# Optimization experiments

Measured on AMD Instinct MI355X. Metric: run time of the kernel, lower is better.

The kernel has to match this reference:

```python
import jax, jax.numpy as jnp
import numpy as np

B, N, D, D_OUT = 8, 2048, 256, 256
LN_EPS = 1e-5
LRELU_SLOPE = 0.01


def setup_inputs() -> dict:
    key = jax.random.key(0)
    ks = jax.random.split(key, 11)
    s_in = 1.0 / np.sqrt(D)
    s_out = 1.0 / np.sqrt(D)
    return {
        "x_local": jax.random.normal(ks[0], (B, N, D), dtype=jnp.float32),
        "Wq": jax.random.uniform(ks[1], (D, D), jnp.float32, -s_in, s_in),
        "bq": jax.random.uniform(ks[2], (D,), jnp.float32, -s_in, s_in),
        "Wk": jax.random.uniform(ks[3], (D, D), jnp.float32, -s_in, s_in),
        "bk": jax.random.uniform(ks[4], (D,), jnp.float32, -s_in, s_in),
        "Wv": jax.random.uniform(ks[5], (D, D), jnp.float32, -s_in, s_in),
        "bv": jax.random.uniform(ks[6], (D,), jnp.float32, -s_in, s_in),
        "Wo": jax.random.uniform(ks[7], (D_OUT, D), jnp.float32, -s_out, s_out),
        "bo": jax.random.uniform(ks[8], (D_OUT,), jnp.float32, -s_out, s_out),
        "ln_gamma": jnp.ones((D_OUT,), jnp.float32),
        "ln_beta": jnp.zeros((D_OUT,), jnp.float32),
    }


def reference(x_local, Wq, bq, Wk, bk, Wv, bv, Wo, bo, ln_gamma, ln_beta):
    # Linear layers (torch convention: y = x @ W.T + b)
    Q = jnp.einsum("bnd,ed->bne", x_local, Wq) + bq
    K = jnp.einsum("bnd,ed->bne", x_local, Wk) + bk
    V = jnp.einsum("bnd,ed->bne", x_local, Wv) + bv
    # Unscaled attention (source applies no 1/sqrt(d))
    scores = jnp.einsum("bnd,bmd->bnm", Q, K)          # [B, N, N]
    attn = jax.nn.softmax(scores, axis=-1)
    loc = jnp.einsum("bnm,bmd->bnd", attn, V)           # [B, N, D]
    # fc_out: Linear -> LayerNorm -> LeakyReLU
    h = jnp.einsum("bnd,ed->bne", loc, Wo) + bo          # [B, N, D_OUT]
    mu = jnp.mean(h, axis=-1, keepdims=True)
    var = jnp.mean(jnp.square(h - mu), axis=-1, keepdims=True)
    hn = (h - mu) / jnp.sqrt(var + LN_EPS) * ln_gamma + ln_beta
    return jnp.where(hn >= 0, hn, LRELU_SLOPE * hn)
```

## Files before the change

### kernel.cpp

```cpp
#include <hip/hip_runtime.h>

typedef unsigned short u16;
typedef __attribute__((ext_vector_type(8))) _Float16 f16x8;
typedef __attribute__((ext_vector_type(4))) float f32x4;

#define MFMA_F16 __builtin_amdgcn_mfma_f32_16x16x32_f16

static __device__ __forceinline__ u16 f2h(float f) {
    return __builtin_bit_cast(u16, (_Float16)f);
}
static __device__ __forceinline__ ushort4 f4_to_h4(const float4 v) {
    ushort4 r;
    r.x = f2h(v.x); r.y = f2h(v.y); r.z = f2h(v.z); r.w = f2h(v.w);
    return r;
}

__global__ __launch_bounds__(256) void prep_w(
    const float* __restrict__ wq, const float* __restrict__ wk,
    const float* __restrict__ wv, const float* __restrict__ wo,
    u16* __restrict__ w4)
{
    const int tid = blockIdx.x * 256 + threadIdx.x;
    for (int i = tid; i < 65536; i += 16384) {
        const float* src = (i < 16384) ? wq : (i < 32768) ? wk
                         : (i < 49152) ? wv : wo;
        ((ushort4*)w4)[i] = f4_to_h4(((const float4*)src)[i & 16383]);
    }
}

__global__ __launch_bounds__(256) void proj_qkv(
    const float* __restrict__ X, const u16* __restrict__ w4,
    const float* __restrict__ bq, const float* __restrict__ bk,
    const float* __restrict__ bv,
    u16* __restrict__ Qh, u16* __restrict__ Kh, u16* __restrict__ Vt)
{
    const int z = blockIdx.y;
    const u16* __restrict__ W     = w4 + z * 65536;
    const float* __restrict__ bias = (z == 0) ? bq : (z == 1) ? bk : bv;

    const int m0   = blockIdx.x * 64;
    const int t    = threadIdx.x;
    const int w    = t >> 6;
    const int lane = t & 63;
    const int quad = lane >> 4;
    const int l16  = lane & 15;

    __shared__ __align__(16) u16 smem[18432];
    u16* Xs = smem;
    u16* Ws = smem + 2560;

    f32x4 acc[16];
#pragma unroll
    for (int i = 0; i < 16; ++i) acc[i] = f32x4{0.f, 0.f, 0.f, 0.f};

    for (int kc = 0; kc < 8; ++kc) {
#pragma unroll
        for (int i = 0; i < 2; ++i) {
            const int ch = i * 256 + t;
            const int row = ch >> 3, cg = ch & 7;
            const float4 v = *(const float4*)&X[(size_t)(m0 + row) * 256 + kc * 32 + cg * 4];
            *(ushort4*)&Xs[row * 40 + cg * 4] = f4_to_h4(v);
        }
#pragma unroll
        for (int i = 0; i < 4; ++i) {
            const int ch = i * 256 + t;
            const int row = ch >> 2, cg = ch & 3;
            *(int4*)&Ws[row * 40 + cg * 8] =
                *(const int4*)&W[(size_t)row * 256 + kc * 32 + cg * 8];
        }
        __syncthreads();

        const f16x8 af = *(const f16x8*)&Xs[(w * 16 + l16) * 40 + quad * 8];
#pragma unroll
        for (int nt = 0; nt < 16; ++nt) {
            const f16x8 bf = *(const f16x8*)&Ws[(nt * 16 + l16) * 40 + quad * 8];
            acc[nt] = MFMA_F16(af, bf, acc[nt], 0, 0, 0);
        }
        __syncthreads();
    }

    if (z < 2) {
        u16* __restrict__ Y = (z == 0) ? Qh : Kh;
#pragma unroll
        for (int nt = 0; nt < 16; ++nt) {
            const int col = nt * 16 + l16;
            const float bb = bias[col];
#pragma unroll
            for (int r = 0; r < 4; ++r)
                smem[(w * 16 + quad * 4 + r) * 264 + col] = f2h(acc[nt][r] + bb);
        }
        __syncthreads();
#pragma unroll
        for (int i = 0; i < 8; ++i) {
            const int ch = i * 256 + t;
            const int row = ch >> 5, cg = ch & 31;
            *(int4*)&Y[(size_t)(m0 + row) * 256 + cg * 8] =
                *(const int4*)&smem[row * 264 + cg * 8];
        }
    } else {
        const int b  = m0 >> 11;
        const int n0 = m0 & 2047;
#pragma unroll
        for (int nt = 0; nt < 16; ++nt) {
            const int col = nt * 16 + l16;
            const float bb = bias[col];
            ushort4 h4;
            h4.x = f2h(acc[nt][0] + bb);
            h4.y = f2h(acc[nt][1] + bb);
            h4.z = f2h(acc[nt][2] + bb);
            h4.w = f2h(acc[nt][3] + bb);
            *(ushort4*)&smem[col * 72 + w * 16 + quad * 4] = h4;
        }
        __syncthreads();
#pragma unroll
        for (int i = 0; i < 8; ++i) {
            const int ch = i * 256 + t;
            const int row = ch >> 3, cg = ch & 7;
            *(int4*)&Vt[(size_t)b * 524288 + (size_t)row * 2048 + n0 + cg * 8] =
                *(const int4*)&smem[row * 72 + cg * 8];
        }
    }
}

__global__ __launch_bounds__(256) void attn(
    const u16* __restrict__ Qh, const u16* __restrict__ Kg,
    const u16* __restrict__ Vt, u16* __restrict__ Op, float* __restrict__ lmp)
{
    const int nz = gridDim.z;
    const int z  = blockIdx.z;
    const int tbase = 64 / nz, trem = 64 % nz;
    const int my_tiles = tbase + (z < trem ? 1 : 0);
    const int tile0    = tbase * z + (z < trem ? z : trem);

    const int b  = blockIdx.y;
    const int q0 = blockIdx.x * 64;
    const int t    = threadIdx.x;
    const int w    = t >> 6;
    const int lane = t & 63;
    const int quad = lane >> 4;
    const int l16  = lane & 15;

    __shared__ __align__(16) u16 smem[18688];
    u16* Ks = smem;
    u16* Vs = smem + 8448;
    u16* Os = smem;

    f16x8 qf[8];
    {
        const size_t qrow = (size_t)(b * 2048 + q0 + w * 16 + l16) * 256;
#pragma unroll
        for (int kc = 0; kc < 8; ++kc)
            qf[kc] = *(const f16x8*)&Qh[qrow + kc * 32 + quad * 8];
    }

    f32x4 O[16];
#pragma unroll
    for (int i = 0; i < 16; ++i) O[i] = f32x4{0.f, 0.f, 0.f, 0.f};
    float mrow = -1e30f, lrow = 0.f;

    for (int it = 0; it < my_tiles; ++it) {
        const int kt = (tile0 + it) * 32;
#pragma unroll
        for (int i = 0; i < 4; ++i) {
            const int ch = i * 256 + t;
            const int row = ch >> 5, cg = ch & 31;
            const int prow = ((row >> 2) & 3) * 8 + (row >> 4) * 4 + (row & 3);
            *(int4*)&Ks[row * 264 + cg * 8] =
                *(const int4*)&Kg[(size_t)(b * 2048 + kt + prow) * 256 + cg * 8];
        }
#pragma unroll
        for (int i = 0; i < 4; ++i) {
            const int ch = i * 256 + t;
            const int row = ch >> 2, cg = ch & 3;
            *(int4*)&Vs[row * 40 + cg * 8] =
                *(const int4*)&Vt[(size_t)b * 524288 + (size_t)row * 2048 + kt + cg * 8];
        }
        __syncthreads();

        f32x4 S[2];
        S[0] = f32x4{0.f, 0.f, 0.f, 0.f};
        S[1] = f32x4{0.f, 0.f, 0.f, 0.f};
#pragma unroll
        for (int kc = 0; kc < 8; ++kc) {
#pragma unroll
            for (int kn = 0; kn < 2; ++kn) {
                const f16x8 kf = *(const f16x8*)&Ks[(kn * 16 + l16) * 264 + kc * 32 + quad * 8];
                S[kn] = MFMA_F16(kf, qf[kc], S[kn], 0, 0, 0);
            }
        }

        float mt = fmaxf(fmaxf(fmaxf(S[0][0], S[0][1]), fmaxf(S[0][2], S[0][3])),
                         fmaxf(fmaxf(S[1][0], S[1][1]), fmaxf(S[1][2], S[1][3])));
        mt = fmaxf(mt, __shfl_xor(mt, 16));
        mt = fmaxf(mt, __shfl_xor(mt, 32));
        const float mnew = fmaxf(mrow, mt);
        const float a = __expf(mrow - mnew);
        float p[2][4];
        float s = 0.f;
#pragma unroll
        for (int kn = 0; kn < 2; ++kn)
#pragma unroll
            for (int r = 0; r < 4; ++r) {
                p[kn][r] = __expf(S[kn][r] - mnew);
                s += p[kn][r];
            }
        s += __shfl_xor(s, 16);
        s += __shfl_xor(s, 32);
        lrow = a * lrow + s;
        mrow = mnew;

        if (__any(a < 1.f)) {
#pragma unroll
            for (int dv = 0; dv < 16; ++dv)
#pragma unroll
                for (int r = 0; r < 4; ++r) O[dv][r] *= a;
        }

        f16x8 pf;
#pragma unroll
        for (int kn = 0; kn < 2; ++kn)
#pragma unroll
            for (int r = 0; r < 4; ++r)
                pf[kn * 4 + r] = (_Float16)p[kn][r];

#pragma unroll
        for (int dvt = 0; dvt < 16; ++dvt) {
            const f16x8 vf = *(const f16x8*)&Vs[(dvt * 16 + l16) * 40 + quad * 8];
            O[dvt] = MFMA_F16(vf, pf, O[dvt], 0, 0, 0);
        }
        __syncthreads();
    }

    {
        const float rl = 1.0f / lrow;
#pragma unroll
        for (int dvt = 0; dvt < 16; ++dvt) {
            ushort4 h4;
            h4.x = f2h(O[dvt][0] * rl);
            h4.y = f2h(O[dvt][1] * rl);
            h4.z = f2h(O[dvt][2] * rl);
            h4.w = f2h(O[dvt][3] * rl);
            *(ushort4*)&Os[(w * 16 + l16) * 264 + dvt * 16 + quad * 4] = h4;
        }
        if (quad == 0) {
            const int grow = b * 2048 + q0 + w * 16 + l16;
            lmp[z * 16384 + grow]        = lrow;
            lmp[(nz + z) * 16384 + grow] = mrow;
        }
    }
    __syncthreads();

    u16* __restrict__ Oz = Op + (size_t)z * 4194304;
    {
        const int row = t >> 2;
#pragma unroll
        for (int i = 0; i < 8; ++i) {
            const int chunk = (t & 3) * 8 + i;
            *(int4*)&Oz[(size_t)(b * 2048 + q0 + row) * 256 + chunk * 8] =
                *(const int4*)&Os[row * 264 + chunk * 8];
        }
    }
}

__global__ __launch_bounds__(256) void outproj_ln(
    const u16* __restrict__ Op, const float* __restrict__ lmp,
    const u16* __restrict__ Woh, const float* __restrict__ bo,
    const float* __restrict__ gamma, const float* __restrict__ beta,
    float* __restrict__ out)
{
    const int m0   = blockIdx.x * 64;
    const int t    = threadIdx.x;
    const int w    = t >> 6;
    const int lane = t & 63;
    const int quad = lane >> 4;
    const int l16  = lane & 15;

    __shared__ __align__(16) u16 Ls[64 * 40];
    __shared__ __align__(16) u16 Ws[256 * 40];
    __shared__ _Float16 w0s[64], w1s[64];

    if (t < 64) {
        const float l0 = lmp[m0 + t],          l1 = lmp[16384 + m0 + t];
        const float mm0 = lmp[32768 + m0 + t], mm1 = lmp[49152 + m0 + t];
        const float mm = fmaxf(mm0, mm1);
        const float u0 = l0 * __expf(mm0 - mm);
        const float u1 = l1 * __expf(mm1 - mm);
        const float inv = 1.0f / (u0 + u1);
        w0s[t] = (_Float16)(u0 * inv);
        w1s[t] = (_Float16)(u1 * inv);
    }
    __syncthreads();

    f32x4 acc[16];
#pragma unroll
    for (int i = 0; i < 16; ++i) acc[i] = f32x4{0.f, 0.f, 0.f, 0.f};

    for (int kc = 0; kc < 8; ++kc) {
        {
            const int row = t >> 2, cg = t & 3;
            const size_t off = (size_t)(m0 + row) * 256 + kc * 32 + cg * 8;
            const f16x8 o0 = __builtin_bit_cast(f16x8, *(const int4*)&Op[off]);
            const f16x8 o1 = __builtin_bit_cast(f16x8, *(const int4*)&Op[4194304 + off]);
            const _Float16 w0 = w0s[row], w1 = w1s[row];
            f16x8 lw;
#pragma unroll
            for (int j = 0; j < 8; ++j) lw[j] = o0[j] * w0 + o1[j] * w1;
            *(int4*)&Ls[row * 40 + cg * 8] = __builtin_bit_cast(int4, lw);
        }
#pragma unroll
        for (int i = 0; i < 4; ++i) {
            const int ch = i * 256 + t;
            const int row = ch >> 2, cg = ch & 3;
            *(int4*)&Ws[row * 40 + cg * 8] =
                *(const int4*)&Woh[(size_t)row * 256 + kc * 32 + cg * 8];
        }
        __syncthreads();

        const f16x8 af = *(const f16x8*)&Ls[(w * 16 + l16) * 40 + quad * 8];
#pragma unroll
        for (int nt = 0; nt < 16; ++nt) {
            const f16x8 bf = *(const f16x8*)&Ws[(nt * 16 + l16) * 40 + quad * 8];
            acc[nt] = MFMA_F16(af, bf, acc[nt], 0, 0, 0);
        }
        __syncthreads();
    }

    float g[16], bt[16], bb[16];
#pragma unroll
    for (int nt = 0; nt < 16; ++nt) {
        const int col = nt * 16 + l16;
        bb[nt] = bo[col]; g[nt] = gamma[col]; bt[nt] = beta[col];
    }

#pragma unroll
    for (int r = 0; r < 4; ++r) {
        float h[16];
        float sh = 0.f, sh2 = 0.f;
#pragma unroll
        for (int nt = 0; nt < 16; ++nt) {
            h[nt] = acc[nt][r] + bb[nt];
            sh  += h[nt];
            sh2 += h[nt] * h[nt];
        }
        sh  += __shfl_xor(sh, 1);  sh  += __shfl_xor(sh, 2);
        sh  += __shfl_xor(sh, 4);  sh  += __shfl_xor(sh, 8);
        sh2 += __shfl_xor(sh2, 1); sh2 += __shfl_xor(sh2, 2);
        sh2 += __shfl_xor(sh2, 4); sh2 += __shfl_xor(sh2, 8);
        const float mu  = sh * (1.f / 256.f);
        const float var = fmaxf(sh2 * (1.f / 256.f) - mu * mu, 0.f);
        const float rs  = rsqrtf(var + 1e-5f);
        const size_t row = (size_t)(m0 + w * 16 + quad * 4 + r) * 256;
#pragma unroll
        for (int nt = 0; nt < 16; ++nt) {
            const float hn = (h[nt] - mu) * rs * g[nt] + bt[nt];
            out[row + nt * 16 + l16] = (hn >= 0.f) ? hn : 0.01f * hn;
        }
    }
}

extern "C" void kernel_launch(void* const* d_in, const int* in_sizes, int n_in,
                              void* d_out, int out_size, void* d_ws, size_t ws_size,
                              hipStream_t stream)
{
    const float* x  = (const float*)d_in[0];
    const float* Wq = (const float*)d_in[1];
    const float* bq = (const float*)d_in[2];
    const float* Wk = (const float*)d_in[3];
    const float* bk = (const float*)d_in[4];
    const float* Wv = (const float*)d_in[5];
    const float* bv = (const float*)d_in[6];
    const float* Wo = (const float*)d_in[7];
    const float* bo = (const float*)d_in[8];
    const float* gm = (const float*)d_in[9];
    const float* bt = (const float*)d_in[10];
    float* out = (float*)d_out;

    u16* W4 = (u16*)d_ws;
    u16* Qh = W4 + 262144;
    u16* Kh = Qh + 4194304;
    u16* Vt = Kh + 4194304;
    u16* Op = Vt + 4194304;
    float* lmp = (float*)(Op + 2 * 4194304);
    u16* Woh = W4 + 196608;

    prep_w     <<<64,             256, 0, stream>>>(Wq, Wk, Wv, Wo, W4);
    proj_qkv   <<<dim3(256, 3),   256, 0, stream>>>(x, W4, bq, bk, bv, Qh, Kh, Vt);
    attn       <<<dim3(32, 8, 2), 256, 0, stream>>>(Qh, Kh, Vt, Op, lmp);
    outproj_ln <<<256,            256, 0, stream>>>(Op, lmp, Woh, bo, gm, bt, out);
}
```

Baseline: 201.8 us.

## Fuse weight fp16 conversion into GEMM loads and halve out-projection row tile

Drops the separate prep_w kernel. The projection and out-projection kernels now read fp32 weights directly and convert them to fp16 while staging into shared memory, which removes one launch and a workspace round trip. The out-projection kernel now uses 32-row tiles with waves split across column halves, so it launches twice as many blocks. LayerNorm statistics are combined through shared memory partial sums. The cost is twice the global weight bytes per block, with that load repeated by every block, plus an extra barrier.

```diff
diff --git a/kernel.cpp b/kernel.cpp
--- a/kernel.cpp
+++ b/kernel.cpp
@@ -15,27 +15,16 @@
     return r;
 }
 
-__global__ __launch_bounds__(256) void prep_w(
+__global__ __launch_bounds__(256) void proj_qkv(
+    const float* __restrict__ X,
     const float* __restrict__ wq, const float* __restrict__ wk,
-    const float* __restrict__ wv, const float* __restrict__ wo,
-    u16* __restrict__ w4)
-{
-    const int tid = blockIdx.x * 256 + threadIdx.x;
-    for (int i = tid; i < 65536; i += 16384) {
-        const float* src = (i < 16384) ? wq : (i < 32768) ? wk
-                         : (i < 49152) ? wv : wo;
-        ((ushort4*)w4)[i] = f4_to_h4(((const float4*)src)[i & 16383]);
-    }
-}
-
-__global__ __launch_bounds__(256) void proj_qkv(
-    const float* __restrict__ X, const u16* __restrict__ w4,
+    const float* __restrict__ wv,
     const float* __restrict__ bq, const float* __restrict__ bk,
     const float* __restrict__ bv,
     u16* __restrict__ Qh, u16* __restrict__ Kh, u16* __restrict__ Vt)
 {
     const int z = blockIdx.y;
-    const u16* __restrict__ W     = w4 + z * 65536;
+    const float* __restrict__ W    = (z == 0) ? wq : (z == 1) ? wk : wv;
     const float* __restrict__ bias = (z == 0) ? bq : (z == 1) ? bk : bv;
 
     const int m0   = blockIdx.x * 64;
@@ -62,11 +51,11 @@
             *(ushort4*)&Xs[row * 40 + cg * 4] = f4_to_h4(v);
         }
 #pragma unroll
-        for (int i = 0; i < 4; ++i) {
-            const int ch = i * 256 + t;
-            const int row = ch >> 2, cg = ch & 3;
-            *(int4*)&Ws[row * 40 + cg * 8] =
-                *(const int4*)&W[(size_t)row * 256 + kc * 32 + cg * 8];
+        for (int i = 0; i < 8; ++i) {
+            const int ch = i * 256 + t;
+            const int row = ch >> 3, cg = ch & 7;
+            const float4 v = *(const float4*)&W[(size_t)row * 256 + kc * 32 + cg * 4];
+            *(ushort4*)&Ws[row * 40 + cg * 4] = f4_to_h4(v);
         }
         __syncthreads();
 
@@ -264,22 +253,25 @@
 
 __global__ __launch_bounds__(256) void outproj_ln(
     const u16* __restrict__ Op, const float* __restrict__ lmp,
-    const u16* __restrict__ Woh, const float* __restrict__ bo,
+    const float* __restrict__ Wo, const float* __restrict__ bo,
     const float* __restrict__ gamma, const float* __restrict__ beta,
     float* __restrict__ out)
 {
-    const int m0   = blockIdx.x * 64;
+    const int m0   = blockIdx.x * 32;
     const int t    = threadIdx.x;
     const int w    = t >> 6;
+    const int rh   = w >> 1;
+    const int chf  = w & 1;
     const int lane = t & 63;
     const int quad = lane >> 4;
     const int l16  = lane & 15;
 
-    __shared__ __align__(16) u16 Ls[64 * 40];
+    __shared__ __align__(16) u16 Ls[32 * 40];
     __shared__ __align__(16) u16 Ws[256 * 40];
-    __shared__ _Float16 w0s[64], w1s[64];
-
-    if (t < 64) {
+    __shared__ _Float16 w0s[32], w1s[32];
+    __shared__ float psum[2][32], psum2[2][32];
+
+    if (t < 32) {
         const float l0 = lmp[m0 + t],          l1 = lmp[16384 + m0 + t];
         const float mm0 = lmp[32768 + m0 + t], mm1 = lmp[49152 + m0 + t];
         const float mm = fmaxf(mm0, mm1);
@@ -291,12 +283,12 @@
     }
     __syncthreads();
 
-    f32x4 acc[16];
-#pragma unroll
-    for (int i = 0; i < 16; ++i) acc[i] = f32x4{0.f, 0.f, 0.f, 0.f};
+    f32x4 acc[8];
+#pragma unroll
+    for (int i = 0; i < 8; ++i) acc[i] = f32x4{0.f, 0.f, 0.f, 0.f};
 
     for (int kc = 0; kc < 8; ++kc) {
-        {
+        if (t < 128) {
             const int row = t >> 2, cg = t & 3;
             const size_t off = (size_t)(m0 + row) * 256 + kc * 32 + cg * 8;
             const f16x8 o0 = __builtin_bit_cast(f16x8, *(const int4*)&Op[off]);
@@ -308,52 +300,64 @@
             *(int4*)&Ls[row * 40 + cg * 8] = __builtin_bit_cast(int4, lw);
         }
 #pragma unroll
-        for (int i = 0; i < 4; ++i) {
-            const int ch = i * 256 + t;
-            const int row = ch >> 2, cg = ch & 3;
-            *(int4*)&Ws[row * 40 + cg * 8] =
-                *(const int4*)&Woh[(size_t)row * 256 + kc * 32 + cg * 8];
-        }
-        __syncthreads();
-
-        const f16x8 af = *(const f16x8*)&Ls[(w * 16 + l16) * 40 + quad * 8];
-#pragma unroll
-        for (int nt = 0; nt < 16; ++nt) {
-            const f16x8 bf = *(const f16x8*)&Ws[(nt * 16 + l16) * 40 + quad * 8];
+        for (int i = 0; i < 8; ++i) {
+            const int ch = i * 256 + t;
+            const int row = ch >> 3, cg = ch & 7;
+            const float4 v = *(const float4*)&Wo[(size_t)row * 256 + kc * 32 + cg * 4];
+            *(ushort4*)&Ws[row * 40 + cg * 4] = f4_to_h4(v);
+        }
+        __syncthreads();
+
+        const f16x8 af = *(const f16x8*)&Ls[(rh * 16 + l16) * 40 + quad * 8];
+#pragma unroll
+        for (int nt = 0; nt < 8; ++nt) {
+            const f16x8 bf = *(const f16x8*)&Ws[(chf * 128 + nt * 16 + l16) * 40 + quad * 8];
             acc[nt] = MFMA_F16(af, bf, acc[nt], 0, 0, 0);
         }
         __syncthreads();
     }
 
-    float g[16], bt[16], bb[16];
-#pragma unroll
-    for (int nt = 0; nt < 16; ++nt) {
-        const int col = nt * 16 + l16;
+    float g[8], bt[8], bb[8];
+#pragma unroll
+    for (int nt = 0; nt < 8; ++nt) {
+        const int col = chf * 128 + nt * 16 + l16;
         bb[nt] = bo[col]; g[nt] = gamma[col]; bt[nt] = beta[col];
     }
 
+    float h[8][4];
 #pragma unroll
     for (int r = 0; r < 4; ++r) {
-        float h[16];
         float sh = 0.f, sh2 = 0.f;
 #pragma unroll
-        for (int nt = 0; nt < 16; ++nt) {
-            h[nt] = acc[nt][r] + bb[nt];
-            sh  += h[nt];
-            sh2 += h[nt] * h[nt];
+        for (int nt = 0; nt < 8; ++nt) {
+            h[nt][r] = acc[nt][r] + bb[nt];
+            sh  += h[nt][r];
+            sh2 += h[nt][r] * h[nt][r];
         }
         sh  += __shfl_xor(sh, 1);  sh  += __shfl_xor(sh, 2);
         sh  += __shfl_xor(sh, 4);  sh  += __shfl_xor(sh, 8);
         sh2 += __shfl_xor(sh2, 1); sh2 += __shfl_xor(sh2, 2);
         sh2 += __shfl_xor(sh2, 4); sh2 += __shfl_xor(sh2, 8);
+        if (l16 == 0) {
+            psum [chf][rh * 16 + quad * 4 + r] = sh;
+            psum2[chf][rh * 16 + quad * 4 + r] = sh2;
+        }
+    }
+    __syncthreads();
+
+#pragma unroll
+    for (int r = 0; r < 4; ++r) {
+        const int row32 = rh * 16 + quad * 4 + r;
+        const float sh  = psum [0][row32] + psum [1][row32];
+        const float sh2 = psum2[0][row32] + psum2[1][row32];
         const float mu  = sh * (1.f / 256.f);
         const float var = fmaxf(sh2 * (1.f / 256.f) - mu * mu, 0.f);
         const float rs  = rsqrtf(var + 1e-5f);
-        const size_t row = (size_t)(m0 + w * 16 + quad * 4 + r) * 256;
-#pragma unroll
-        for (int nt = 0; nt < 16; ++nt) {
-            const float hn = (h[nt] - mu) * rs * g[nt] + bt[nt];
-            out[row + nt * 16 + l16] = (hn >= 0.f) ? hn : 0.01f * hn;
+        const size_t row = (size_t)(m0 + row32) * 256;
+#pragma unroll
+        for (int nt = 0; nt < 8; ++nt) {
+            const float hn = (h[nt][r] - mu) * rs * g[nt] + bt[nt];
+            out[row + chf * 128 + nt * 16 + l16] = (hn >= 0.f) ? hn : 0.01f * hn;
         }
     }
 }
@@ -375,16 +379,13 @@
     const float* bt = (const float*)d_in[10];
     float* out = (float*)d_out;
 
-    u16* W4 = (u16*)d_ws;
-    u16* Qh = W4 + 262144;
+    u16* Qh = (u16*)d_ws;
     u16* Kh = Qh + 4194304;
     u16* Vt = Kh + 4194304;
     u16* Op = Vt + 4194304;
     float* lmp = (float*)(Op + 2 * 4194304);
-    u16* Woh = W4 + 196608;
-
-    prep_w     <<<64,             256, 0, stream>>>(Wq, Wk, Wv, Wo, W4);
-    proj_qkv   <<<dim3(256, 3),   256, 0, stream>>>(x, W4, bq, bk, bv, Qh, Kh, Vt);
+
+    proj_qkv   <<<dim3(256, 3),   256, 0, stream>>>(x, Wq, Wk, Wv, bq, bk, bv, Qh, Kh, Vt);
     attn       <<<dim3(32, 8, 2), 256, 0, stream>>>(Qh, Kh, Vt, Op, lmp);
-    outproj_ln <<<256,            256, 0, stream>>>(Op, lmp, Woh, bo, gm, bt, out);
-}
+    outproj_ln <<<512,            256, 0, stream>>>(Op, lmp, Wo, bo, gm, bt, out);
+}
```

New measurement: 212.4 us. +5.2%, slower.
